# Performance work log

Hardware: AMD Instinct MI355X
Metric: run time of the kernel (lower is better)

Reference implementation:

```python
import jax, jax.numpy as jnp
import numpy as np

WAY = 5
SHOT = 5
SCALE = 10.0
EPS = 1e-8


def setup_inputs() -> dict:
    key = jax.random.key(0)
    k1, k2 = jax.random.split(key, 2)
    x = jax.random.normal(k1, (100, 512, 16, 16), dtype=jnp.float32)
    W = jax.random.normal(k2, (512, 512), dtype=jnp.float32) * 0.02  # 1x1 conv weight (outC, inC)
    b = jnp.zeros((512,), dtype=jnp.float32)
    return {"x": x, "W": W, "b": b}


def reference(x, W, b):
    B, C, H, Wd = x.shape
    # extract(): 1x1 conv -> softmax over flattened (C*H*W) per sample -> remask
    mask = jnp.einsum('bchw,oc->bohw', x, W) + b[None, :, None, None]
    mask = jax.nn.softmax(mask.reshape(B, -1), axis=1).reshape(B, C, H, Wd)
    x = x * mask
    # predict(): (way, shot+query, C, H, W)
    xv = x.reshape(WAY, -1, C, H, Wd)
    s = xv[:, :SHOT].mean(axis=(1, 3, 4))                    # (m=way, d=C) support prototypes
    q = xv[:, SHOT:].reshape(-1, C, H * Wd)                  # (n, d=C, f=H*W) queries
    # cosine_similarity over d, without materializing (n,m,d,f)
    qn = jnp.maximum(jnp.sqrt(jnp.sum(q * q, axis=1)), EPS)  # (n, f)
    sn = jnp.maximum(jnp.sqrt(jnp.sum(s * s, axis=1)), EPS)  # (m,)
    scores = jnp.einsum('ndf,md->nmf', q, s) / (qn[:, None, :] * sn[None, :, None])
    # softmax over classes (m), then mean over spatial positions f
    return jax.nn.softmax(SCALE * scores, axis=1).mean(axis=2)  # (n, way)
```

## Files before the change

kernel.cpp:

```cpp
#include <hip/hip_runtime.h>
#include <hip/hip_bf16.h>
#include <math.h>

typedef _Float16 half8 __attribute__((ext_vector_type(8)));
typedef float f32x4 __attribute__((ext_vector_type(4)));

#define BATCH 100
#define CH    512
#define HWP   256
#define SAMP  (CH * HWP)

__device__ __forceinline__ void async16(const void* g, void* l) {
  __builtin_amdgcn_global_load_lds(
      (const __attribute__((address_space(1))) unsigned int*)g,
      (__attribute__((address_space(3))) unsigned int*)l, 16, 0, 0);
}

__global__ __launch_bounds__(256) void k_txpose(const float* __restrict__ x,
                                               _Float16* __restrict__ xh,
                                               const float* __restrict__ W,
                                               _Float16* __restrict__ Wh,
                                               float* __restrict__ denom,
                                               float* __restrict__ raw) {
  __shared__ float tb[64][69];
  int bid  = blockIdx.x;
  if (bid >= 3200) {
    int base = (bid - 3200) * 1024 + threadIdx.x;
#pragma unroll
    for (int j = 0; j < 4; j++) Wh[base + j * 256] = (_Float16)W[base + j * 256];
    if (bid == 3200 && threadIdx.x < 128) denom[threadIdx.x] = 0.0f;
    if (bid >= 3201 && bid < 3251) {
      int rb = (bid - 3201) * 1024 + threadIdx.x;
#pragma unroll
      for (int j = 0; j < 4; j++) raw[rb + j * 256] = 0.0f;
    }
    return;
  }
  int b    = bid >> 5;
  int tile = bid & 31;
  int c0 = (tile >> 2) << 6;
  int p0 = (tile & 3) << 6;
  int t = threadIdx.x;
  const float* xb = x + (size_t)b * SAMP;
#pragma unroll
  for (int it = 0; it < 4; it++) {
    int ch = it * 256 + t;
    int c  = ch >> 4;
    int pc = (ch & 15) << 2;
    float4 v = *(const float4*)(xb + (size_t)(c0 + c) * HWP + p0 + pc);
    tb[c][pc] = v.x; tb[c][pc + 1] = v.y; tb[c][pc + 2] = v.z; tb[c][pc + 3] = v.w;
  }
  __syncthreads();
  _Float16* xhb = xh + (size_t)b * SAMP;
#pragma unroll
  for (int it = 0; it < 2; it++) {
    int ch = it * 256 + t;
    int p  = ch >> 3;
    int ck = (ch & 7) << 3;
    half8 h;
#pragma unroll
    for (int j = 0; j < 8; j++) h[j] = (_Float16)tb[ck + j][p];
    *(half8*)(xhb + (size_t)(p0 + p) * CH + c0 + ck) = h;
  }
}

__global__ __launch_bounds__(256) void k_gemm(const _Float16* __restrict__ Wh,
                                             const _Float16* __restrict__ xh,
                                             const float* __restrict__ bias,
                                             _Float16* __restrict__ u,
                                             float* __restrict__ denom,
                                             float* __restrict__ raw) {
  __shared__ __align__(16) _Float16 smem[128 * 136];
  int bid = blockIdx.x;
  int w     = (bid & 7) * 100 + (bid >> 3);
  int batch = w >> 3;
  int sub   = w & 7;
  int ot = sub & 3, pt = sub >> 2;
  int o0 = ot * 128, p0 = pt * 128;
  const _Float16* Bg = xh + (size_t)batch * SAMP;

  int t  = threadIdx.x;
  int wv = t >> 6, ln = t & 63;
  int qd = ln >> 4, r = ln & 15;
  int wm0 = (wv >> 1) * 64, wn0 = (wv & 1) * 64;

  auto stage = [&](int q, int kk) {
    _Float16* As = smem + q * 8192;
    _Float16* Bs = As + 4096;
#pragma unroll
    for (int it = 0; it < 2; it++) {
      int ch  = it * 256 + t;
      int row = ch >> 2;
      int qc  = ch & 3;
      char* la = (char*)As + (size_t)(it * 256 + wv * 64) * 16;
      char* lb = (char*)Bs + (size_t)(it * 256 + wv * 64) * 16;
      async16((const char*)(Wh + (size_t)(o0 + row) * 512 + kk + qc * 8), la);
      async16((const char*)(Bg + (size_t)(p0 + row) * 512 + kk + qc * 8), lb);
    }
  };

  f32x4 acc[4][4] = {};
  stage(0, 0);

  for (int ks = 0; ks < 16; ks++) {
    int q = ks & 1;
    if (ks < 15) {
      stage(q ^ 1, (ks + 1) * 32);
      asm volatile("s_waitcnt vmcnt(4)" ::: "memory");
    } else {
      asm volatile("s_waitcnt vmcnt(0)" ::: "memory");
    }
    __builtin_amdgcn_s_barrier();
    asm volatile("" ::: "memory");
    const _Float16* As = smem + q * 8192;
    const _Float16* Bs = As + 4096;
    half8 af[4], bf[4];
#pragma unroll
    for (int i = 0; i < 4; i++)
      af[i] = *(const half8*)(As + (wm0 + i * 16 + r) * 32 + qd * 8);
#pragma unroll
    for (int j = 0; j < 4; j++)
      bf[j] = *(const half8*)(Bs + (wn0 + j * 16 + r) * 32 + qd * 8);
#pragma unroll
    for (int i = 0; i < 4; i++)
#pragma unroll
      for (int j = 0; j < 4; j++)
        acc[i][j] = __builtin_amdgcn_mfma_f32_16x16x32_f16(af[i], bf[j], acc[i][j], 0, 0, 0);
    asm volatile("" ::: "memory");
    __builtin_amdgcn_s_barrier();
  }

#pragma unroll
  for (int it = 0; it < 8; it++) {
    int ch = it * 256 + t;
    int p  = ch >> 4;
    int ck = ch & 15;
    half8 v = *(const half8*)(Bg + (size_t)(p0 + p) * CH + o0 + ck * 8);
    *(half8*)(smem + p * 136 + ck * 8) = v;
  }
  __syncthreads();

  bool is_supp = (batch % 20) < 5;
  _Float16* outb = u + (size_t)batch * SAMP;
  float lsum = 0.f;
  if (!is_supp) {
#pragma unroll
    for (int i = 0; i < 4; i++) {
#pragma unroll
      for (int rg = 0; rg < 4; rg++) {
        int ol = wm0 + i * 16 + qd * 4 + rg;
        float bv = bias[o0 + ol];
#pragma unroll
        for (int j = 0; j < 4; j++) {
          int pl = wn0 + j * 16 + r;
          float ev = __expf(acc[i][j][rg] + bv);
          lsum += ev;
          float xv = (float)smem[pl * 136 + ol];
          outb[(size_t)(o0 + ol) * HWP + p0 + pl] = (_Float16)(xv * ev);
        }
      }
    }
  } else {
    float* rawb = raw + (size_t)batch * 512 + o0;
#pragma unroll
    for (int i = 0; i < 4; i++) {
#pragma unroll
      for (int rg = 0; rg < 4; rg++) {
        int ol = wm0 + i * 16 + qd * 4 + rg;
        float bv = bias[o0 + ol];
        float s4 = 0.f;
#pragma unroll
        for (int j = 0; j < 4; j++) {
          int pl = wn0 + j * 16 + r;
          float ev = __expf(acc[i][j][rg] + bv);
          lsum += ev;
          float xv = (float)smem[pl * 136 + ol];
          s4 += xv * ev;
        }
#pragma unroll
        for (int off = 1; off < 16; off <<= 1) s4 += __shfl_xor(s4, off, 64);
        if (r == 0) atomicAdd(&rawb[ol], s4);
      }
    }
  }
#pragma unroll
  for (int off = 32; off; off >>= 1) lsum += __shfl_down(lsum, off, 64);
  __shared__ float rs[4];
  if (ln == 0) rs[wv] = lsum;
  __syncthreads();
  if (t == 0) atomicAdd(&denom[batch], rs[0] + rs[1] + rs[2] + rs[3]);
}

__global__ __launch_bounds__(256) void k_part(const _Float16* __restrict__ u,
                                             const float* __restrict__ raw,
                                             const float* __restrict__ denom,
                                             float* __restrict__ part) {
  __shared__ float s_l[5 * 64];
  int n = blockIdx.x >> 3, gc = blockIdx.x & 7;
  int b = (n / 15) * 20 + 5 + (n % 15);
  int t = threadIdx.x;
  for (int i = t; i < 320; i += 256) {
    int m = i >> 6, cl = i & 63;
    int c = gc * 64 + cl;
    float s = 0.f;
#pragma unroll
    for (int j = 0; j < 5; j++) {
      int sb = m * 20 + j;
      s += raw[sb * 512 + c] / denom[sb];
    }
    s_l[i] = s * (1.0f / 1280.0f);
  }
  __syncthreads();
  const _Float16* ub = u + (size_t)b * SAMP + (size_t)gc * 64 * HWP;
  float dot[5] = {0, 0, 0, 0, 0}, qq = 0.f;
#pragma unroll 8
  for (int c = 0; c < 64; c++) {
    float v = (float)ub[c * HWP + t];
    qq += v * v;
#pragma unroll
    for (int m = 0; m < 5; m++) dot[m] += v * s_l[m * 64 + c];
  }
  float* pp = part + (size_t)(n * 8 + gc) * 6 * 256 + t;
  pp[0 * 256] = dot[0]; pp[1 * 256] = dot[1]; pp[2 * 256] = dot[2];
  pp[3 * 256] = dot[3]; pp[4 * 256] = dot[4]; pp[5 * 256] = qq;
}

__global__ __launch_bounds__(256) void k_comb(const float* __restrict__ part,
                                             const float* __restrict__ raw,
                                             const float* __restrict__ denom,
                                             float* __restrict__ out) {
  int n = blockIdx.x, t = threadIdx.x;
  int wv = t >> 6;
  __shared__ float prefs[5];
  __shared__ float rsn[4][5];
  {
    float sn2[5];
#pragma unroll
    for (int m = 0; m < 5; m++) {
      float s1 = 0.f, s2 = 0.f;
#pragma unroll
      for (int j = 0; j < 5; j++) {
        int sb = m * 20 + j;
        float inv = 1.0f / denom[sb];
        s1 += raw[sb * 512 + t] * inv;
        s2 += raw[sb * 512 + 256 + t] * inv;
      }
      s1 *= (1.0f / 1280.0f); s2 *= (1.0f / 1280.0f);
      sn2[m] = s1 * s1 + s2 * s2;
    }
#pragma unroll
    for (int m = 0; m < 5; m++) {
      float v = sn2[m];
#pragma unroll
      for (int off = 32; off; off >>= 1) v += __shfl_down(v, off, 64);
      sn2[m] = v;
    }
    if ((t & 63) == 0) {
#pragma unroll
      for (int m = 0; m < 5; m++) rsn[wv][m] = sn2[m];
    }
    __syncthreads();
    if (t < 5) prefs[t] =
        10.0f / fmaxf(sqrtf(rsn[0][t] + rsn[1][t] + rsn[2][t] + rsn[3][t]), 1e-8f);
    __syncthreads();
  }
  float dot[5] = {0, 0, 0, 0, 0}, qq = 0.f;
#pragma unroll
  for (int gc = 0; gc < 8; gc++) {
    const float* pp = part + (size_t)(n * 8 + gc) * 6 * 256 + t;
    dot[0] += pp[0 * 256]; dot[1] += pp[1 * 256]; dot[2] += pp[2 * 256];
    dot[3] += pp[3 * 256]; dot[4] += pp[4 * 256]; qq += pp[5 * 256];
  }
  float iqn = 1.0f / fmaxf(sqrtf(qq), 1e-20f);
  float sc[5], mx = -1e30f;
#pragma unroll
  for (int m = 0; m < 5; m++) { sc[m] = dot[m] * prefs[m] * iqn; mx = fmaxf(mx, sc[m]); }
  float p[5], ssum = 0.f;
#pragma unroll
  for (int m = 0; m < 5; m++) { p[m] = __expf(sc[m] - mx); ssum += p[m]; }
  float rr = 1.0f / ssum;
#pragma unroll
  for (int m = 0; m < 5; m++) {
    float v = p[m] * rr;
#pragma unroll
    for (int off = 32; off; off >>= 1) v += __shfl_down(v, off, 64);
    p[m] = v;
  }
  __shared__ float rs[4][5];
  if ((t & 63) == 0) {
#pragma unroll
    for (int m = 0; m < 5; m++) rs[t >> 6][m] = p[m];
  }
  __syncthreads();
  if (t < 5) out[n * 5 + t] =
      (rs[0][t] + rs[1][t] + rs[2][t] + rs[3][t]) * (1.0f / 256.0f);
}

extern "C" void kernel_launch(void* const* d_in, const int* in_sizes, int n_in,
                              void* d_out, int out_size, void* d_ws, size_t ws_size,
                              hipStream_t stream) {
  const float* x    = (const float*)d_in[0];
  const float* W    = (const float*)d_in[1];
  const float* bias = (const float*)d_in[2];
  float* out = (float*)d_out;

  char* ws = (char*)d_ws;
  _Float16* xh     = (_Float16*)(ws + 0);
  float*    part   = (float*)   (ws + 0);
  _Float16* Wh     = (_Float16*)(ws + 26214400);
  _Float16* u      = (_Float16*)(ws + 26738688);
  float*    denom  = (float*)   (ws + 52953088);
  float*    raw    = (float*)   (ws + 52953600);

  k_txpose <<<3456, 256, 0, stream>>>(x, xh, W, Wh, denom, raw);
  k_gemm   <<<800,  256, 0, stream>>>(Wh, xh, bias, u, denom, raw);
  k_part   <<<600,  256, 0, stream>>>(u, raw, denom, part);
  k_comb   <<<75,   256, 0, stream>>>(part, raw, denom, out);
}
```

Measured before the change: 134.7 us.

## Fuse x transpose/fp16 cast into GEMM and replace atomics with partial buffers

The separate transpose kernel that wrote an fp16 transposed copy of x is removed. The GEMM now reads fp32 x directly into registers, converts and transposes it into LDS with software double buffering, and reads fp32 x again in the epilogue. Atomic accumulation of denom and raw is replaced by per-tile partial buffers that downstream kernels sum, which also removes the zeroing pass. This avoids a full write and re-read of the 26MB intermediate, but the GEMM's loads become strided scalar fp32 and synchronous instead of async LDS loads.

New measurement: 138.6 us. +2.9%, slower.

```diff
diff --git a/kernel.cpp b/kernel.cpp
--- a/kernel.cpp
+++ b/kernel.cpp
@@ -3,6 +3,7 @@
 #include <math.h>
 
 typedef _Float16 half8 __attribute__((ext_vector_type(8)));
+typedef _Float16 half4 __attribute__((ext_vector_type(4)));
 typedef float f32x4 __attribute__((ext_vector_type(4)));
 
 #define BATCH 100
@@ -10,108 +11,76 @@
 #define HWP   256
 #define SAMP  (CH * HWP)
 
-__device__ __forceinline__ void async16(const void* g, void* l) {
-  __builtin_amdgcn_global_load_lds(
-      (const __attribute__((address_space(1))) unsigned int*)g,
-      (__attribute__((address_space(3))) unsigned int*)l, 16, 0, 0);
-}
-
-__global__ __launch_bounds__(256) void k_txpose(const float* __restrict__ x,
-                                               _Float16* __restrict__ xh,
-                                               const float* __restrict__ W,
-                                               _Float16* __restrict__ Wh,
-                                               float* __restrict__ denom,
-                                               float* __restrict__ raw) {
-  __shared__ float tb[64][69];
-  int bid  = blockIdx.x;
-  if (bid >= 3200) {
-    int base = (bid - 3200) * 1024 + threadIdx.x;
-#pragma unroll
-    for (int j = 0; j < 4; j++) Wh[base + j * 256] = (_Float16)W[base + j * 256];
-    if (bid == 3200 && threadIdx.x < 128) denom[threadIdx.x] = 0.0f;
-    if (bid >= 3201 && bid < 3251) {
-      int rb = (bid - 3201) * 1024 + threadIdx.x;
-#pragma unroll
-      for (int j = 0; j < 4; j++) raw[rb + j * 256] = 0.0f;
-    }
-    return;
-  }
-  int b    = bid >> 5;
-  int tile = bid & 31;
-  int c0 = (tile >> 2) << 6;
-  int p0 = (tile & 3) << 6;
-  int t = threadIdx.x;
-  const float* xb = x + (size_t)b * SAMP;
-#pragma unroll
-  for (int it = 0; it < 4; it++) {
-    int ch = it * 256 + t;
-    int c  = ch >> 4;
-    int pc = (ch & 15) << 2;
-    float4 v = *(const float4*)(xb + (size_t)(c0 + c) * HWP + p0 + pc);
-    tb[c][pc] = v.x; tb[c][pc + 1] = v.y; tb[c][pc + 2] = v.z; tb[c][pc + 3] = v.w;
-  }
-  __syncthreads();
-  _Float16* xhb = xh + (size_t)b * SAMP;
-#pragma unroll
-  for (int it = 0; it < 2; it++) {
-    int ch = it * 256 + t;
-    int p  = ch >> 3;
-    int ck = (ch & 7) << 3;
-    half8 h;
-#pragma unroll
-    for (int j = 0; j < 8; j++) h[j] = (_Float16)tb[ck + j][p];
-    *(half8*)(xhb + (size_t)(p0 + p) * CH + c0 + ck) = h;
-  }
+__global__ __launch_bounds__(256) void k_convw(const float* __restrict__ W,
+                                              _Float16* __restrict__ Wh) {
+  int base = blockIdx.x * 1024 + threadIdx.x;
+#pragma unroll
+  for (int j = 0; j < 4; j++) Wh[base + j * 256] = (_Float16)W[base + j * 256];
 }
 
 __global__ __launch_bounds__(256) void k_gemm(const _Float16* __restrict__ Wh,
-                                             const _Float16* __restrict__ xh,
+                                             const float* __restrict__ xf,
                                              const float* __restrict__ bias,
                                              _Float16* __restrict__ u,
-                                             float* __restrict__ denom,
-                                             float* __restrict__ raw) {
-  __shared__ __align__(16) _Float16 smem[128 * 136];
+                                             float* __restrict__ denom_part,
+                                             float* __restrict__ raw_part) {
+  __shared__ __align__(16) _Float16 smem[16384];
   int bid = blockIdx.x;
   int w     = (bid & 7) * 100 + (bid >> 3);
   int batch = w >> 3;
   int sub   = w & 7;
   int ot = sub & 3, pt = sub >> 2;
   int o0 = ot * 128, p0 = pt * 128;
-  const _Float16* Bg = xh + (size_t)batch * SAMP;
+  const float* xb = xf + (size_t)batch * SAMP;
 
   int t  = threadIdx.x;
   int wv = t >> 6, ln = t & 63;
   int qd = ln >> 4, r = ln & 15;
   int wm0 = (wv >> 1) * 64, wn0 = (wv & 1) * 64;
-
-  auto stage = [&](int q, int kk) {
+  int c4 = ln >> 3, p0l = ln & 7;
+  int pwb = wv * 32 + p0l;
+
+  half8 areg[2];
+  float breg[4][4];
+
+  auto LOADT = [&](int kk) {
+#pragma unroll
+    for (int it = 0; it < 2; it++) {
+      int ch = it * 256 + t, row = ch >> 2, qc = ch & 3;
+      areg[it] = *(const half8*)(Wh + (size_t)(o0 + row) * 512 + kk + qc * 8);
+    }
+#pragma unroll
+    for (int i = 0; i < 4; i++)
+#pragma unroll
+      for (int k = 0; k < 4; k++)
+        breg[i][k] = xb[(size_t)(kk + c4 * 4 + i) * HWP + p0 + pwb + 8 * k];
+  };
+  auto WRITET = [&](int q) {
     _Float16* As = smem + q * 8192;
     _Float16* Bs = As + 4096;
 #pragma unroll
     for (int it = 0; it < 2; it++) {
-      int ch  = it * 256 + t;
-      int row = ch >> 2;
-      int qc  = ch & 3;
-      char* la = (char*)As + (size_t)(it * 256 + wv * 64) * 16;
-      char* lb = (char*)Bs + (size_t)(it * 256 + wv * 64) * 16;
-      async16((const char*)(Wh + (size_t)(o0 + row) * 512 + kk + qc * 8), la);
-      async16((const char*)(Bg + (size_t)(p0 + row) * 512 + kk + qc * 8), lb);
+      int ch = it * 256 + t, row = ch >> 2, qc = ch & 3;
+      *(half8*)(As + row * 32 + qc * 8) = areg[it];
+    }
+#pragma unroll
+    for (int k = 0; k < 4; k++) {
+      half4 h;
+#pragma unroll
+      for (int i = 0; i < 4; i++) h[i] = (_Float16)breg[i][k];
+      *(half4*)(Bs + (pwb + 8 * k) * 32 + c4 * 4) = h;
     }
   };
 
   f32x4 acc[4][4] = {};
-  stage(0, 0);
+  LOADT(0);
+  WRITET(0);
+  asm volatile("s_waitcnt lgkmcnt(0)" ::: "memory");
+  __builtin_amdgcn_s_barrier();
 
   for (int ks = 0; ks < 16; ks++) {
     int q = ks & 1;
-    if (ks < 15) {
-      stage(q ^ 1, (ks + 1) * 32);
-      asm volatile("s_waitcnt vmcnt(4)" ::: "memory");
-    } else {
-      asm volatile("s_waitcnt vmcnt(0)" ::: "memory");
-    }
-    __builtin_amdgcn_s_barrier();
-    asm volatile("" ::: "memory");
+    if (ks < 15) LOADT((ks + 1) * 32);
     const _Float16* As = smem + q * 8192;
     const _Float16* Bs = As + 4096;
     half8 af[4], bf[4];
@@ -126,79 +95,97 @@
 #pragma unroll
       for (int j = 0; j < 4; j++)
         acc[i][j] = __builtin_amdgcn_mfma_f32_16x16x32_f16(af[i], bf[j], acc[i][j], 0, 0, 0);
-    asm volatile("" ::: "memory");
+    asm volatile("s_waitcnt lgkmcnt(0)" ::: "memory");
     __builtin_amdgcn_s_barrier();
-  }
-
-#pragma unroll
-  for (int it = 0; it < 8; it++) {
-    int ch = it * 256 + t;
-    int p  = ch >> 4;
-    int ck = ch & 15;
-    half8 v = *(const half8*)(Bg + (size_t)(p0 + p) * CH + o0 + ck * 8);
-    *(half8*)(smem + p * 136 + ck * 8) = v;
-  }
-  __syncthreads();
+    if (ks < 15) WRITET(q ^ 1);
+    asm volatile("s_waitcnt lgkmcnt(0)" ::: "memory");
+    __builtin_amdgcn_s_barrier();
+  }
+
+  __syncthreads();
+  float* smr = (float*)smem;
+  float* rs  = ((float*)smem) + 128;
 
   bool is_supp = (batch % 20) < 5;
-  _Float16* outb = u + (size_t)batch * SAMP;
   float lsum = 0.f;
   if (!is_supp) {
+    _Float16* outb = u + (size_t)batch * SAMP;
 #pragma unroll
     for (int i = 0; i < 4; i++) {
 #pragma unroll
       for (int rg = 0; rg < 4; rg++) {
         int ol = wm0 + i * 16 + qd * 4 + rg;
         float bv = bias[o0 + ol];
+        const float* xrow = xb + (size_t)(o0 + ol) * HWP + p0;
+        _Float16* urow = outb + (size_t)(o0 + ol) * HWP + p0;
 #pragma unroll
         for (int j = 0; j < 4; j++) {
           int pl = wn0 + j * 16 + r;
           float ev = __expf(acc[i][j][rg] + bv);
           lsum += ev;
-          float xv = (float)smem[pl * 136 + ol];
-          outb[(size_t)(o0 + ol) * HWP + p0 + pl] = (_Float16)(xv * ev);
+          urow[pl] = (_Float16)(xrow[pl] * ev);
         }
       }
     }
   } else {
-    float* rawb = raw + (size_t)batch * 512 + o0;
+    float s4a[4][4];
 #pragma unroll
     for (int i = 0; i < 4; i++) {
 #pragma unroll
       for (int rg = 0; rg < 4; rg++) {
         int ol = wm0 + i * 16 + qd * 4 + rg;
         float bv = bias[o0 + ol];
+        const float* xrow = xb + (size_t)(o0 + ol) * HWP + p0;
         float s4 = 0.f;
 #pragma unroll
         for (int j = 0; j < 4; j++) {
           int pl = wn0 + j * 16 + r;
           float ev = __expf(acc[i][j][rg] + bv);
           lsum += ev;
-          float xv = (float)smem[pl * 136 + ol];
-          s4 += xv * ev;
+          s4 += xrow[pl] * ev;
         }
 #pragma unroll
         for (int off = 1; off < 16; off <<= 1) s4 += __shfl_xor(s4, off, 64);
-        if (r == 0) atomicAdd(&rawb[ol], s4);
+        s4a[i][rg] = s4;
+        if (wn0 == 0 && r == 0) smr[ol] = s4;
       }
     }
+    __syncthreads();
+    if (wn0 == 64) {
+      float* rp = raw_part + (size_t)(batch * 2 + pt) * 512 + o0;
+#pragma unroll
+      for (int i = 0; i < 4; i++)
+#pragma unroll
+        for (int rg = 0; rg < 4; rg++) {
+          int ol = wm0 + i * 16 + qd * 4 + rg;
+          if (r == 0) rp[ol] = s4a[i][rg] + smr[ol];
+        }
+    }
   }
 #pragma unroll
   for (int off = 32; off; off >>= 1) lsum += __shfl_down(lsum, off, 64);
-  __shared__ float rs[4];
   if (ln == 0) rs[wv] = lsum;
   __syncthreads();
-  if (t == 0) atomicAdd(&denom[batch], rs[0] + rs[1] + rs[2] + rs[3]);
+  if (t == 0) denom_part[batch * 8 + sub] = rs[0] + rs[1] + rs[2] + rs[3];
 }
 
 __global__ __launch_bounds__(256) void k_part(const _Float16* __restrict__ u,
-                                             const float* __restrict__ raw,
-                                             const float* __restrict__ denom,
+                                             const float* __restrict__ raw_part,
+                                             const float* __restrict__ denom_part,
                                              float* __restrict__ part) {
+  __shared__ float sd[25];
   __shared__ float s_l[5 * 64];
   int n = blockIdx.x >> 3, gc = blockIdx.x & 7;
   int b = (n / 15) * 20 + 5 + (n % 15);
   int t = threadIdx.x;
+  if (t < 25) {
+    int sb = (t / 5) * 20 + (t % 5);
+    float d = 0.f;
+#pragma unroll
+    for (int s = 0; s < 8; s++) d += denom_part[sb * 8 + s];
+    sd[t] = 1.0f / d;
+  }
+  __syncthreads();
   for (int i = t; i < 320; i += 256) {
     int m = i >> 6, cl = i & 63;
     int c = gc * 64 + cl;
@@ -206,7 +193,8 @@
 #pragma unroll
     for (int j = 0; j < 5; j++) {
       int sb = m * 20 + j;
-      s += raw[sb * 512 + c] / denom[sb];
+      s += (raw_part[(size_t)(sb * 2) * 512 + c] +
+            raw_part[(size_t)(sb * 2 + 1) * 512 + c]) * sd[m * 5 + j];
     }
     s_l[i] = s * (1.0f / 1280.0f);
   }
@@ -226,13 +214,22 @@
 }
 
 __global__ __launch_bounds__(256) void k_comb(const float* __restrict__ part,
-                                             const float* __restrict__ raw,
-                                             const float* __restrict__ denom,
+                                             const float* __restrict__ raw_part,
+                                             const float* __restrict__ denom_part,
                                              float* __restrict__ out) {
   int n = blockIdx.x, t = threadIdx.x;
   int wv = t >> 6;
+  __shared__ float sd[25];
   __shared__ float prefs[5];
   __shared__ float rsn[4][5];
+  if (t < 25) {
+    int sb = (t / 5) * 20 + (t % 5);
+    float d = 0.f;
+#pragma unroll
+    for (int s = 0; s < 8; s++) d += denom_part[sb * 8 + s];
+    sd[t] = 1.0f / d;
+  }
+  __syncthreads();
   {
     float sn2[5];
 #pragma unroll
@@ -241,9 +238,11 @@
 #pragma unroll
       for (int j = 0; j < 5; j++) {
         int sb = m * 20 + j;
-        float inv = 1.0f / denom[sb];
-        s1 += raw[sb * 512 + t] * inv;
-        s2 += raw[sb * 512 + 256 + t] * inv;
+        float inv = sd[m * 5 + j];
+        s1 += (raw_part[(size_t)(sb * 2) * 512 + t] +
+               raw_part[(size_t)(sb * 2 + 1) * 512 + t]) * inv;
+        s2 += (raw_part[(size_t)(sb * 2) * 512 + 256 + t] +
+               raw_part[(size_t)(sb * 2 + 1) * 512 + 256 + t]) * inv;
       }
       s1 *= (1.0f / 1280.0f); s2 *= (1.0f / 1280.0f);
       sn2[m] = s1 * s1 + s2 * s2;
@@ -305,15 +304,14 @@
   float* out = (float*)d_out;
 
   char* ws = (char*)d_ws;
-  _Float16* xh     = (_Float16*)(ws + 0);
   float*    part   = (float*)   (ws + 0);
-  _Float16* Wh     = (_Float16*)(ws + 26214400);
-  _Float16* u      = (_Float16*)(ws + 26738688);
-  float*    denom  = (float*)   (ws + 52953088);
-  float*    raw    = (float*)   (ws + 52953600);
-
-  k_txpose <<<3456, 256, 0, stream>>>(x, xh, W, Wh, denom, raw);
-  k_gemm   <<<800,  256, 0, stream>>>(Wh, xh, bias, u, denom, raw);
-  k_part   <<<600,  256, 0, stream>>>(u, raw, denom, part);
-  k_comb   <<<75,   256, 0, stream>>>(part, raw, denom, out);
-}
+  _Float16* Wh     = (_Float16*)(ws + 2764800);
+  _Float16* u      = (_Float16*)(ws + 3289088);
+  float*    dpart  = (float*)   (ws + 29503488);
+  float*    rpart  = (float*)   (ws + 29506688);
+
+  k_convw <<<256, 256, 0, stream>>>(W, Wh);
+  k_gemm  <<<800, 256, 0, stream>>>(Wh, x, bias, u, dpart, rpart);
+  k_part  <<<600, 256, 0, stream>>>(u, rpart, dpart, part);
+  k_comb  <<<75,  256, 0, stream>>>(part, rpart, dpart, out);
+}
```
